# Optimization experiments

Hardware: AMD Instinct MI355X
Metric: run time of the kernel (lower is better)

Reference implementation:

```python
import jax, jax.numpy as jnp
import numpy as np

H, BS, NB, R, K = 2048, 128, 44, 64, 8   # hidden, block_size, num_blocks, basis_rank, top_k
B, S = 4, 2048
I = NB * BS                               # intermediate size = 5632


def setup_inputs() -> dict:
    key = jax.random.key(0)
    ks = jax.random.split(key, 10)
    N = B * S
    return {
        "hidden_states": jax.random.normal(ks[0], (B, S, H), jnp.float32),
        "active_idx": jax.random.randint(ks[1], (N, K), 0, NB, jnp.int32),
        "active_score": jax.random.uniform(ks[2], (N, K), dtype=jnp.float32),
        "gate_w": jax.random.normal(ks[3], (I, H), jnp.float32) * 0.02,
        "up_w": jax.random.normal(ks[4], (I, H), jnp.float32) * 0.02,
        "down_w": jax.random.normal(ks[5], (H, I), jnp.float32) * 0.02,
        "enc_w": jax.random.normal(ks[6], (R, H), jnp.float32) * 0.02,
        "enc_b": jnp.zeros((R,), jnp.float32),
        "decoder": jax.random.normal(ks[7], (NB, R, BS), jnp.float32) * 0.02,
        "basis_bias": jnp.zeros((NB, BS), jnp.float32),
        "comp_bias": jnp.zeros((H,), jnp.float32),
        "scale": jnp.array(1.0, jnp.float32),
    }


def reference(hidden_states, active_idx, active_score, gate_w, up_w, down_w,
              enc_w, enc_b, decoder, basis_bias, comp_bias, scale):
    Bb, Ss, Hh = hidden_states.shape
    N = Bb * Ss
    x = hidden_states.reshape(N, Hh)                          # [N, H]

    # routing weights: softmax over selected block scores (all idx valid here),
    # scattered into a dense per-token per-block weight map (duplicates accumulate)
    w = jax.nn.softmax(active_score, axis=-1)                 # [N, K]
    block_w = jnp.zeros((N, NB), x.dtype).at[
        jnp.arange(N)[:, None], active_idx].add(w)            # [N, NB]

    # gated SiLU MLP intermediate over all blocks (dense equivalent of the
    # per-token block gather-compute)
    act = jax.nn.silu(x @ gate_w.T) * (x @ up_w.T)            # [N, I]

    # low-rank basis compensation: latent -> per-block block_size channels
    latent = jax.nn.silu(x @ enc_w.T + enc_b)                 # [N, R]
    comp = jnp.einsum('nr,brc->nbc', latent, decoder) + basis_bias  # [N, NB, BS]

    act_b = act.reshape(N, NB, BS) + scale * comp             # [N, NB, BS]
    weighted = (act_b * block_w[:, :, None]).reshape(N, I)    # mask+weight inactive blocks to 0

    out = weighted @ down_w.T + comp_bias                     # scatter back via down proj
    return out.reshape(Bb, Ss, Hh)
```

## Files before the change

kernel.cpp:

```cpp
#include <hip/hip_runtime.h>

#define H_  2048
#define BS_ 128
#define NB_ 44
#define R_  64
#define K_  8
#define N_  8192
#define I_  5632
#define MT  64
#define TILES 32
#define GRID_AB (8 * 6 * TILES)

typedef __bf16 bf16x8 __attribute__((ext_vector_type(8)));
typedef float  f32x4  __attribute__((ext_vector_type(4)));

__device__ __forceinline__ unsigned short f2bf(float f) {
  unsigned int u = __float_as_uint(f);
  u = (u + 0x7FFFu + ((u >> 16) & 1u)) >> 16;
  return (unsigned short)u;
}
__device__ __forceinline__ float bf2f(unsigned short s) {
  return __uint_as_float(((unsigned int)s) << 16);
}
__device__ __forceinline__ bf16x8 ld8(const unsigned short* p) {
  uint4 v = *reinterpret_cast<const uint4*>(p);
  return __builtin_bit_cast(bf16x8, v);
}
__device__ __forceinline__ bf16x8 lds8(const char* p) {
  uint4 v = *reinterpret_cast<const uint4*>(p);
  return __builtin_bit_cast(bf16x8, v);
}
__device__ __forceinline__ void gl16(const void* g, void* l) {
  __builtin_amdgcn_global_load_lds(
      (const __attribute__((address_space(1))) char*)g,
      (__attribute__((address_space(3))) char*)l, 16, 0, 0);
}
#define WAIT_VM(n) do { asm volatile("s_waitcnt vmcnt(" #n ")" ::: "memory"); \
                        __builtin_amdgcn_sched_barrier(0); } while (0)
#define WAIT_LGKM0 do { asm volatile("s_waitcnt lgkmcnt(0)" ::: "memory"); \
                        __builtin_amdgcn_sched_barrier(0); } while (0)
#define SBAR __builtin_amdgcn_s_barrier()

__global__ void cvt_xgu(const float* __restrict__ x, const float* __restrict__ gw,
                        const float* __restrict__ uw, const float* __restrict__ ew,
                        const float* __restrict__ dw,
                        unsigned short* __restrict__ xb,
                        unsigned short* __restrict__ gwb,
                        unsigned short* __restrict__ uwb,
                        unsigned short* __restrict__ ewb,
                        unsigned short* __restrict__ dwb,
                        int do_down) {
  const int NX4 = N_ * H_ / 4;
  const int NG4 = I_ * H_ / 4;
  const int NE4 = R_ * H_ / 4;
  const int ND4 = H_ * I_ / 4;
  int total = NX4 + 2 * NG4 + NE4 + (do_down ? ND4 : 0);
  int stride = gridDim.x * blockDim.x;
  for (int i = blockIdx.x * blockDim.x + threadIdx.x; i < total; i += stride) {
    if (i < NX4 + 2 * NG4 + NE4) {
      const float4* s; ushort4* d; int j;
      if (i < NX4)                  { s = (const float4*)x;  d = (ushort4*)xb;  j = i; }
      else if (i < NX4 + NG4)       { s = (const float4*)gw; d = (ushort4*)gwb; j = i - NX4; }
      else if (i < NX4 + 2 * NG4)   { s = (const float4*)uw; d = (ushort4*)uwb; j = i - NX4 - NG4; }
      else                          { s = (const float4*)ew; d = (ushort4*)ewb; j = i - NX4 - 2 * NG4; }
      float4 v = s[j];
      ushort4 o; o.x = f2bf(v.x); o.y = f2bf(v.y); o.z = f2bf(v.z); o.w = f2bf(v.w);
      d[j] = o;
    } else {
      int j = i - (NX4 + 2 * NG4 + NE4);
      float4 v = ((const float4*)dw)[j];
      int flat = j * 4;
      int h = flat / I_;
      int rem = flat - h * I_;
      int b = rem >> 7, k = rem & 127;
      ushort4 o; o.x = f2bf(v.x); o.y = f2bf(v.y); o.z = f2bf(v.z); o.w = f2bf(v.w);
      *(ushort4*)(dwb + ((size_t)b * H_ + h) * BS_ + k) = o;
    }
  }
}

__global__ void cvt_down(const float* __restrict__ dw, unsigned short* __restrict__ dwb) {
  int total = H_ * I_ / 4;
  int stride = gridDim.x * blockDim.x;
  for (int i = blockIdx.x * blockDim.x + threadIdx.x; i < total; i += stride) {
    float4 v = ((const float4*)dw)[i];
    int flat = i * 4;
    int h = flat / I_;
    int rem = flat - h * I_;
    int b = rem >> 7, k = rem & 127;
    ushort4 o; o.x = f2bf(v.x); o.y = f2bf(v.y); o.z = f2bf(v.z); o.w = f2bf(v.w);
    *(ushort4*)(dwb + ((size_t)b * H_ + h) * BS_ + k) = o;
  }
}

__global__ void cvt_dec(const float* __restrict__ dec, unsigned short* __restrict__ decb) {
  int i = blockIdx.x * 256 + threadIdx.x;
  if (i >= NB_ * BS_ * R_) return;
  int b = i >> 13;
  int rem = i & 8191;
  int c = rem >> 6, r = rem & 63;
  decb[i] = f2bf(dec[(b << 13) + r * BS_ + c]);
}

__global__ void zero_counts(int* __restrict__ counts) {
  if (threadIdx.x < NB_) counts[threadIdx.x] = 0;
}

__global__ void prep_kernel(const float* __restrict__ score,
                            const int* __restrict__ aidx,
                            float* __restrict__ w_buf,
                            int* __restrict__ counts) {
  __shared__ int hist[NB_];
  int tid = threadIdx.x;
  if (tid < NB_) hist[tid] = 0;
  __syncthreads();
  int n = blockIdx.x * 256 + tid;
  float s[K_];
  float m = -1e30f;
#pragma unroll
  for (int k = 0; k < K_; k++) { s[k] = score[n * K_ + k]; m = fmaxf(m, s[k]); }
  float sum = 0.f;
#pragma unroll
  for (int k = 0; k < K_; k++) { s[k] = __expf(s[k] - m); sum += s[k]; }
  float inv = 1.f / sum;
#pragma unroll
  for (int k = 0; k < K_; k++) {
    w_buf[n * K_ + k] = s[k] * inv;
    atomicAdd(&hist[aidx[n * K_ + k]], 1);
  }
  __syncthreads();
  if (tid < NB_) atomicAdd(&counts[tid], hist[tid]);
}

__global__ void scan_kernel(const int* __restrict__ counts,
                            int* __restrict__ offsets,
                            int* __restrict__ cursors) {
  if (threadIdx.x == 0) {
    int acc = 0;
    for (int b = 0; b < NB_; b++) { offsets[b] = acc; cursors[b] = acc; acc += counts[b]; }
    offsets[NB_] = acc;
  }
}

__global__ void fill_kernel(const int* __restrict__ aidx,
                            const float* __restrict__ w_buf,
                            int* __restrict__ cursors,
                            int* __restrict__ tok_list,
                            float* __restrict__ wt_list,
                            int* __restrict__ inv) {
  int n = blockIdx.x * 256 + threadIdx.x;
#pragma unroll
  for (int k = 0; k < K_; k++) {
    int b = aidx[n * K_ + k];
    int pos = atomicAdd(&cursors[b], 1);
    tok_list[pos] = n;
    wt_list[pos] = w_buf[n * K_ + k];
    inv[n * K_ + k] = pos;
  }
}

__global__ __launch_bounds__(256) void latent_mfma(
    const unsigned short* __restrict__ xb,
    const unsigned short* __restrict__ ewb,
    const float* __restrict__ enc_b,
    unsigned short* __restrict__ lat) {
  __shared__ __align__(16) char smem[16384];
  int tid = threadIdx.x;
  int wv = tid >> 6, lane = tid & 63;
  int lo = lane & 15, hi = lane >> 4;
  int n0 = blockIdx.x * 64;

  int rowA = tid >> 2;
  int jA = (tid & 3) ^ ((rowA >> 1) & 3);
  const unsigned short* srcA = xb + (size_t)(n0 + rowA) * H_ + jA * 8;
  const unsigned short* srcB = ewb + (size_t)rowA * H_ + jA * 8;

  gl16(srcA, smem + wv * 1024);
  gl16(srcB, smem + 8192 + wv * 1024);

  f32x4 acc[4] = {};
  int cur = 0;
  for (int ks = 0; ks < H_; ks += 32) {
    if (ks + 32 < H_) {
      gl16(srcA + ks + 32, smem + (cur ^ 1) * 4096 + wv * 1024);
      gl16(srcB + ks + 32, smem + 8192 + (cur ^ 1) * 4096 + wv * 1024);
      WAIT_VM(2);
    } else {
      WAIT_VM(0);
    }
    SBAR;
    int rB = wv * 16 + lo;
    bf16x8 Bf = lds8(smem + 8192 + cur * 4096 + (rB * 4 + (hi ^ ((rB >> 1) & 3))) * 16);
#pragma unroll
    for (int m = 0; m < 4; m++) {
      int row = m * 16 + lo;
      bf16x8 Af = lds8(smem + cur * 4096 + (row * 4 + (hi ^ ((row >> 1) & 3))) * 16);
      acc[m] = __builtin_amdgcn_mfma_f32_16x16x32_bf16(Af, Bf, acc[m], 0, 0, 0);
    }
    WAIT_LGKM0;
    SBAR;
    cur ^= 1;
  }

  int r = wv * 16 + lo;
  float eb = enc_b[r];
#pragma unroll
  for (int m = 0; m < 4; m++) {
#pragma unroll
    for (int rg = 0; rg < 4; rg++) {
      int tok = n0 + m * 16 + hi * 4 + rg;
      float v = acc[m][rg] + eb;
      lat[(size_t)tok * R_ + r] = f2bf(v / (1.f + __expf(-v)));
    }
  }
}

__device__ __forceinline__ bool decode_bt(int p, int& b, int& tile) {
  b = (p & 7) + 8 * ((p >> 3) / TILES);
  tile = (p >> 3) % TILES;
  return b < NB_;
}

__global__ __launch_bounds__(256, 4) void gateup_kernel(
    const unsigned short* __restrict__ xb,
    const unsigned short* __restrict__ gwb,
    const unsigned short* __restrict__ uwb,
    const unsigned short* __restrict__ latb,
    const unsigned short* __restrict__ decb_all,
    const float* __restrict__ bbias,
    const float* __restrict__ scale_p,
    const int* __restrict__ counts,
    const int* __restrict__ offsets,
    const int* __restrict__ tok_list,
    const float* __restrict__ wt_list,
    unsigned short* __restrict__ actw) {
  int b, tile;
  if (!decode_bt(blockIdx.x, b, tile)) return;
  int cnt = counts[b];
  int base = tile * MT;
  if (base >= cnt) return;
  int off = offsets[b];

  __shared__ __align__(16) char smem[40960];

  int tid = threadIdx.x;
  int wv = tid >> 6, lane = tid & 63;
  int lo = lane & 15, hi = lane >> 4;

  int rowA = tid >> 2;
  int jA = (tid & 3) ^ ((rowA >> 1) & 3);
  int tokA = tok_list[off + min(base + rowA, cnt - 1)];
  const unsigned short* srcA = xb + (size_t)tokA * H_ + jA * 8;

  const unsigned short* gb = gwb + (size_t)b * BS_ * H_;
  const unsigned short* ub = uwb + (size_t)b * BS_ * H_;
  const unsigned short* srcG[2];
  const unsigned short* srcU[2];
#pragma unroll
  for (int s = 0; s < 2; s++) {
    int o = s * 256 + tid;
    int c = o >> 2;
    int j = (o & 3) ^ ((c >> 1) & 3);
    size_t e = (size_t)c * H_ + j * 8;
    srcG[s] = gb + e;
    srcU[s] = ub + e;
  }

  f32x4 accG[4][2] = {};
  f32x4 accU[4][2] = {};

  gl16(srcA, smem + wv * 1024);
#pragma unroll
  for (int s = 0; s < 2; s++) {
    gl16(srcG[s], smem + 8192 + s * 4096 + wv * 1024);
    gl16(srcU[s], smem + 24576 + s * 4096 + wv * 1024);
  }

  int cur = 0;
  for (int ks = 0; ks < H_; ks += 32) {
    if (ks + 32 < H_) {
      int nb_ = cur ^ 1;
      gl16(srcA + ks + 32, smem + nb_ * 4096 + wv * 1024);
#pragma unroll
      for (int s = 0; s < 2; s++) {
        gl16(srcG[s] + ks + 32, smem + 8192 + nb_ * 8192 + s * 4096 + wv * 1024);
        gl16(srcU[s] + ks + 32, smem + 24576 + nb_ * 8192 + s * 4096 + wv * 1024);
      }
      WAIT_VM(5);
    } else {
      WAIT_VM(0);
    }
    SBAR;
    bf16x8 Af[4];
#pragma unroll
    for (int m = 0; m < 4; m++) {
      int row = m * 16 + lo;
      int off16 = row * 4 + (hi ^ ((row >> 1) & 3));
      Af[m] = lds8(smem + cur * 4096 + off16 * 16);
    }
    bf16x8 Gf[2], Uf[2];
#pragma unroll
    for (int cf = 0; cf < 2; cf++) {
      int c = wv * 32 + cf * 16 + lo;
      int off16 = c * 4 + (hi ^ ((c >> 1) & 3));
      Gf[cf] = lds8(smem + 8192 + cur * 8192 + off16 * 16);
      Uf[cf] = lds8(smem + 24576 + cur * 8192 + off16 * 16);
    }
#pragma unroll
    for (int m = 0; m < 4; m++) {
#pragma unroll
      for (int cf = 0; cf < 2; cf++) {
        accG[m][cf] = __builtin_amdgcn_mfma_f32_16x16x32_bf16(Af[m], Gf[cf], accG[m][cf], 0, 0, 0);
        accU[m][cf] = __builtin_amdgcn_mfma_f32_16x16x32_bf16(Af[m], Uf[cf], accU[m][cf], 0, 0, 0);
      }
    }
    WAIT_LGKM0;
    SBAR;
    cur ^= 1;
  }

#pragma unroll
  for (int s = 0; s < 2; s++) {
    int o = s * 256 + tid;
    int r_ = o >> 3;
    int j = (o & 7) ^ (r_ & 7);
    int tokL = tok_list[off + min(base + r_, cnt - 1)];
    gl16(latb + (size_t)tokL * R_ + j * 8, smem + 24576 + s * 4096 + wv * 1024);
  }
  const unsigned short* decb = decb_all + (size_t)b * BS_ * R_;
#pragma unroll
  for (int s = 0; s < 4; s++) {
    int o = s * 256 + tid;
    int c = o >> 3;
    int j = (o & 7) ^ (c & 7);
    gl16(decb + (size_t)c * R_ + j * 8, smem + 8192 + s * 4096 + wv * 1024);
  }
  __syncthreads();

  f32x4 accC[4][2] = {};
#pragma unroll
  for (int kk = 0; kk < 2; kk++) {
    bf16x8 L[4];
#pragma unroll
    for (int m = 0; m < 4; m++) {
      int row = m * 16 + lo;
      int off16 = row * 8 + ((kk * 4 + hi) ^ (lo & 7));
      L[m] = lds8(smem + 24576 + off16 * 16);
    }
#pragma unroll
    for (int cf = 0; cf < 2; cf++) {
      int c = wv * 32 + cf * 16 + lo;
      int off16 = c * 8 + ((kk * 4 + hi) ^ (lo & 7));
      bf16x8 D = lds8(smem + 8192 + off16 * 16);
#pragma unroll
      for (int m = 0; m < 4; m++)
        accC[m][cf] = __builtin_amdgcn_mfma_f32_16x16x32_bf16(L[m], D, accC[m][cf], 0, 0, 0);
    }
  }

  float scal = scale_p[0];
  int cc[2] = { wv * 32 + lo, wv * 32 + 16 + lo };
  float bbv[2] = { bbias[b * BS_ + cc[0]], bbias[b * BS_ + cc[1]] };
#pragma unroll
  for (int m = 0; m < 4; m++) {
#pragma unroll
    for (int r = 0; r < 4; r++) {
      int t = m * 16 + hi * 4 + r;
      int g = base + t;
      if (g < cnt) {
        float wt = wt_list[off + g];
        unsigned short* dst = actw + (size_t)(off + g) * BS_;
#pragma unroll
        for (int cf = 0; cf < 2; cf++) {
          float gg = accG[m][cf][r];
          float uu = accU[m][cf][r];
          float act = (gg / (1.f + __expf(-gg))) * uu;
          dst[cc[cf]] = f2bf((act + scal * (accC[m][cf][r] + bbv[cf])) * wt);
        }
      }
    }
  }
}

__global__ __launch_bounds__(256) void down_kernel(
    const unsigned short* __restrict__ actw,
    const unsigned short* __restrict__ dwb,
    const int* __restrict__ counts,
    const int* __restrict__ offsets,
    unsigned short* __restrict__ partial,
    int hc0, int Hc) {
  int b, tile;
  if (!decode_bt(blockIdx.x, b, tile)) return;
  int cnt = counts[b];
  int base = tile * MT;
  if (base >= cnt) return;
  int off = offsets[b];

  __shared__ __align__(16) unsigned short a_lds[MT * BS_];
  __shared__ __align__(16) char b_lds[2][16384];
  int tid = threadIdx.x;
  int wv = tid >> 6, lane = tid & 63;
  int lo = lane & 15, hi = lane >> 4;

  for (int i = tid; i < MT * BS_ / 8; i += 256) {
    int t = i >> 4, cb = i & 15;
    int g = base + t;
    uint4 v = make_uint4(0, 0, 0, 0);
    if (g < cnt) v = *(const uint4*)(actw + (size_t)(off + g) * BS_ + cb * 8);
    *(uint4*)(&a_lds[t * BS_ + ((cb ^ (t & 7)) << 3)]) = v;
  }
  __syncthreads();

  bf16x8 Bf[4][4];
#pragma unroll
  for (int kst = 0; kst < 4; kst++)
#pragma unroll
    for (int sf = 0; sf < 4; sf++) {
      int t = sf * 16 + lo, cb = kst * 4 + hi;
      Bf[kst][sf] = ld8(&a_lds[t * BS_ + ((cb ^ (t & 7)) << 3)]);
    }

  const unsigned short* db = dwb + (size_t)b * H_ * BS_;
  int rs = tid >> 4;
  int jc = tid & 15;
  {
    const unsigned short* d0 = db + (size_t)hc0 * BS_;
#pragma unroll
    for (int s = 0; s < 4; s++) {
      int r = s * 16 + rs;
      int j = jc ^ (r & 15);
      gl16(d0 + (size_t)r * BS_ + j * 8, b_lds[0] + s * 4096 + wv * 1024);
    }
  }
  __syncthreads();

  int nit = Hc >> 6;
  int cur = 0;
  for (int it = 0; it < nit; it++) {
    if (it + 1 < nit) {
      const unsigned short* dn = db + (size_t)(hc0 + (it + 1) * 64) * BS_;
#pragma unroll
      for (int s = 0; s < 4; s++) {
        int r = s * 16 + rs;
        int j = jc ^ (r & 15);
        gl16(dn + (size_t)r * BS_ + j * 8, b_lds[cur ^ 1] + s * 4096 + wv * 1024);
      }
    }
    f32x4 acc[4] = {};
    int rl = wv * 16 + lo;
#pragma unroll
    for (int kst = 0; kst < 4; kst++) {
      int cb = kst * 4 + hi;
      bf16x8 Aw = lds8(b_lds[cur] + (rl * 16 + (cb ^ lo)) * 16);
#pragma unroll
      for (int sf = 0; sf < 4; sf++)
        acc[sf] = __builtin_amdgcn_mfma_f32_16x16x32_bf16(Aw, Bf[kst][sf], acc[sf], 0, 0, 0);
    }
    int hrel = it * 64 + wv * 16 + hi * 4;
#pragma unroll
    for (int sf = 0; sf < 4; sf++) {
      int g = base + sf * 16 + lo;
      if (g < cnt) {
        uint2 pk;
        pk.x = (unsigned int)f2bf(acc[sf][0]) | ((unsigned int)f2bf(acc[sf][1]) << 16);
        pk.y = (unsigned int)f2bf(acc[sf][2]) | ((unsigned int)f2bf(acc[sf][3]) << 16);
        *(uint2*)(partial + (size_t)(off + g) * Hc + hrel) = pk;
      }
    }
    __syncthreads();
    cur ^= 1;
  }
}

__global__ __launch_bounds__(256) void reduce_kernel(
    const unsigned short* __restrict__ partial,
    const int* __restrict__ inv,
    const float* __restrict__ cbias,
    float* __restrict__ out, int hc0, int Hc) {
  int wv = threadIdx.x >> 6, l = threadIdx.x & 63;
  int n = blockIdx.x * 4 + wv;
  int rows[K_];
#pragma unroll
  for (int k = 0; k < K_; k++) rows[k] = inv[n * K_ + k];
  for (int c0w = 0; c0w < Hc; c0w += 512) {
    int cw = c0w + l * 8;
    if (cw >= Hc) continue;
    float a[8] = {0.f, 0.f, 0.f, 0.f, 0.f, 0.f, 0.f, 0.f};
#pragma unroll
    for (int k = 0; k < K_; k++) {
      uint4 v = *(const uint4*)(partial + (size_t)rows[k] * Hc + cw);
      unsigned int w0 = v.x, w1 = v.y, w2 = v.z, w3 = v.w;
      a[0] += __uint_as_float(w0 << 16); a[1] += __uint_as_float(w0 & 0xFFFF0000u);
      a[2] += __uint_as_float(w1 << 16); a[3] += __uint_as_float(w1 & 0xFFFF0000u);
      a[4] += __uint_as_float(w2 << 16); a[5] += __uint_as_float(w2 & 0xFFFF0000u);
      a[6] += __uint_as_float(w3 << 16); a[7] += __uint_as_float(w3 & 0xFFFF0000u);
    }
    int h = hc0 + cw;
    float4 c0 = *(const float4*)(cbias + h);
    float4 c1 = *(const float4*)(cbias + h + 4);
    float4 o0 = make_float4(a[0] + c0.x, a[1] + c0.y, a[2] + c0.z, a[3] + c0.w);
    float4 o1 = make_float4(a[4] + c1.x, a[5] + c1.y, a[6] + c1.z, a[7] + c1.w);
    *(float4*)(out + (size_t)n * H_ + h) = o0;
    *(float4*)(out + (size_t)n * H_ + h + 4) = o1;
  }
}

extern "C" void kernel_launch(void* const* d_in, const int* in_sizes, int n_in,
                              void* d_out, int out_size, void* d_ws, size_t ws_size,
                              hipStream_t stream) {
  const float* x       = (const float*)d_in[0];
  const int*   aidx    = (const int*)d_in[1];
  const float* score   = (const float*)d_in[2];
  const float* gate_w  = (const float*)d_in[3];
  const float* up_w    = (const float*)d_in[4];
  const float* down_w  = (const float*)d_in[5];
  const float* enc_w   = (const float*)d_in[6];
  const float* enc_b   = (const float*)d_in[7];
  const float* decoder = (const float*)d_in[8];
  const float* bbias   = (const float*)d_in[9];
  const float* cbias   = (const float*)d_in[10];
  const float* scale   = (const float*)d_in[11];
  float* out = (float*)d_out;

  char* ws = (char*)d_ws;
  const size_t OFF_GWB  = 33554432ull;
  const size_t OFF_UWB  = 56623104ull;
  const size_t OFF_DEC  = 79691776ull;
  const size_t OFF_LATB = 80412672ull;
  const size_t OFF_ENCB = 81461248ull;
  const size_t OFF_WBUF = 81723392ull;
  const size_t OFF_TOK  = 81985536ull;
  const size_t OFF_WT   = 82247680ull;
  const size_t OFF_INV  = 82509824ull;
  const size_t OFF_CNT  = 82771968ull;
  const size_t OFF_ACTW = 82772992ull;
  const size_t BASE_END = 99550208ull;
  const size_t DWB_SZ   = 23068672ull;

  unsigned short* xb   = (unsigned short*)(ws);
  unsigned short* gwb  = (unsigned short*)(ws + OFF_GWB);
  unsigned short* uwb  = (unsigned short*)(ws + OFF_UWB);
  unsigned short* decb = (unsigned short*)(ws + OFF_DEC);
  unsigned short* latb = (unsigned short*)(ws + OFF_LATB);
  unsigned short* ewb  = (unsigned short*)(ws + OFF_ENCB);
  float* w_buf         = (float*)(ws + OFF_WBUF);
  int*   tok_list      = (int*)(ws + OFF_TOK);
  float* wt_list       = (float*)(ws + OFF_WT);
  int*   inv           = (int*)(ws + OFF_INV);
  int*   counts        = (int*)(ws + OFF_CNT);
  int*   offsets       = counts + 64;
  int*   cursors       = counts + 128;
  unsigned short* actw = (unsigned short*)(ws + OFF_ACTW);

  int Hc; unsigned short* dwb; unsigned short* partial; bool early_down;
  if      (ws_size >= BASE_END + DWB_SZ + 131072ull * 512) Hc = 512;
  else if (ws_size >= BASE_END + DWB_SZ + 131072ull * 256) Hc = 256;
  else Hc = 0;
  if (Hc) {
    early_down = true;
    dwb = (unsigned short*)(ws + BASE_END);
    partial = (unsigned short*)(ws + BASE_END + DWB_SZ);
  } else {
    early_down = false;
    Hc = 256;
    dwb = gwb;
    partial = (unsigned short*)ws;
  }
  int nch = H_ / Hc;

  cvt_xgu<<<2048, 256, 0, stream>>>(x, gate_w, up_w, enc_w, down_w,
                                    xb, gwb, uwb, ewb, dwb, early_down ? 1 : 0);
  cvt_dec<<<(NB_ * BS_ * R_ + 255) / 256, 256, 0, stream>>>(decoder, decb);
  zero_counts<<<1, 64, 0, stream>>>(counts);
  prep_kernel<<<N_ / 256, 256, 0, stream>>>(score, aidx, w_buf, counts);
  scan_kernel<<<1, 64, 0, stream>>>(counts, offsets, cursors);
  fill_kernel<<<N_ / 256, 256, 0, stream>>>(aidx, w_buf, cursors, tok_list, wt_list, inv);
  latent_mfma<<<N_ / 64, 256, 0, stream>>>(xb, ewb, enc_b, latb);
  gateup_kernel<<<GRID_AB, 256, 0, stream>>>(xb, gwb, uwb, latb, decb, bbias, scale,
                                             counts, offsets, tok_list, wt_list, actw);
  if (!early_down) cvt_down<<<2048, 256, 0, stream>>>(down_w, dwb);
  for (int c = 0; c < nch; c++) {
    down_kernel<<<GRID_AB, 256, 0, stream>>>(actw, dwb, counts, offsets, partial, c * Hc, Hc);
    reduce_kernel<<<N_ / 4, 256, 0, stream>>>(partial, inv, cbias, out, c * Hc, Hc);
  }
}
```

Before: 575.1 us.

## Triple-buffer activation tile in gate/up loop and allow larger down-proj chunk

The gate/up GEMM loop now keeps three LDS buffers for the gathered activation rows and prefetches them two K-steps ahead, while the weight tiles stay double-buffered. The aim is to hide the latency of the scattered token-row loads behind more MFMA work. This grows LDS per block and lowers the launch-bounds occupancy hint from 4 to 3 blocks. Separately, the host now picks a 1024-wide down-projection chunk when the workspace is large enough, which may change the partial-buffer layout and how much work each pass covers.

```diff
diff --git a/kernel.cpp b/kernel.cpp
--- a/kernel.cpp
+++ b/kernel.cpp
@@ -221,7 +221,7 @@
   return b < NB_;
 }
 
-__global__ __launch_bounds__(256, 4) void gateup_kernel(
+__global__ __launch_bounds__(256, 3) void gateup_kernel(
     const unsigned short* __restrict__ xb,
     const unsigned short* __restrict__ gwb,
     const unsigned short* __restrict__ uwb,
@@ -241,7 +241,7 @@
   if (base >= cnt) return;
   int off = offsets[b];
 
-  __shared__ __align__(16) char smem[40960];
+  __shared__ __align__(16) char smem[45056];
 
   int tid = threadIdx.x;
   int wv = tid >> 6, lane = tid & 63;
@@ -269,22 +269,31 @@
   f32x4 accG[4][2] = {};
   f32x4 accU[4][2] = {};
 
+#pragma unroll
+  for (int s = 0; s < 2; s++) {
+    gl16(srcG[s], smem + 12288 + s * 4096 + wv * 1024);
+    gl16(srcU[s], smem + 28672 + s * 4096 + wv * 1024);
+  }
   gl16(srcA, smem + wv * 1024);
-#pragma unroll
-  for (int s = 0; s < 2; s++) {
-    gl16(srcG[s], smem + 8192 + s * 4096 + wv * 1024);
-    gl16(srcU[s], smem + 24576 + s * 4096 + wv * 1024);
-  }
-
-  int cur = 0;
-  for (int ks = 0; ks < H_; ks += 32) {
-    if (ks + 32 < H_) {
-      int nb_ = cur ^ 1;
-      gl16(srcA + ks + 32, smem + nb_ * 4096 + wv * 1024);
+  gl16(srcA + 32, smem + 4096 + wv * 1024);
+
+  int acur = 0, awr = 2;
+  for (int it = 0; it < 64; ++it) {
+    int ks = it * 32;
+    if (it < 62) {
+      int gu = (it + 1) & 1;
 #pragma unroll
       for (int s = 0; s < 2; s++) {
-        gl16(srcG[s] + ks + 32, smem + 8192 + nb_ * 8192 + s * 4096 + wv * 1024);
-        gl16(srcU[s] + ks + 32, smem + 24576 + nb_ * 8192 + s * 4096 + wv * 1024);
+        gl16(srcG[s] + ks + 32, smem + 12288 + gu * 8192 + s * 4096 + wv * 1024);
+        gl16(srcU[s] + ks + 32, smem + 28672 + gu * 8192 + s * 4096 + wv * 1024);
+      }
+      gl16(srcA + ks + 64, smem + awr * 4096 + wv * 1024);
+      WAIT_VM(6);
+    } else if (it == 62) {
+#pragma unroll
+      for (int s = 0; s < 2; s++) {
+        gl16(srcG[s] + ks + 32, smem + 12288 + 8192 + s * 4096 + wv * 1024);
+        gl16(srcU[s] + ks + 32, smem + 28672 + 8192 + s * 4096 + wv * 1024);
       }
       WAIT_VM(5);
     } else {
@@ -296,15 +305,16 @@
     for (int m = 0; m < 4; m++) {
       int row = m * 16 + lo;
       int off16 = row * 4 + (hi ^ ((row >> 1) & 3));
-      Af[m] = lds8(smem + cur * 4096 + off16 * 16);
+      Af[m] = lds8(smem + acur * 4096 + off16 * 16);
     }
     bf16x8 Gf[2], Uf[2];
+    int gub = it & 1;
 #pragma unroll
     for (int cf = 0; cf < 2; cf++) {
       int c = wv * 32 + cf * 16 + lo;
       int off16 = c * 4 + (hi ^ ((c >> 1) & 3));
-      Gf[cf] = lds8(smem + 8192 + cur * 8192 + off16 * 16);
-      Uf[cf] = lds8(smem + 24576 + cur * 8192 + off16 * 16);
+      Gf[cf] = lds8(smem + 12288 + gub * 8192 + off16 * 16);
+      Uf[cf] = lds8(smem + 28672 + gub * 8192 + off16 * 16);
     }
 #pragma unroll
     for (int m = 0; m < 4; m++) {
@@ -316,7 +326,8 @@
     }
     WAIT_LGKM0;
     SBAR;
-    cur ^= 1;
+    acur = (acur == 2) ? 0 : acur + 1;
+    awr  = (awr  == 2) ? 0 : awr  + 1;
   }
 
 #pragma unroll
@@ -325,7 +336,7 @@
     int r_ = o >> 3;
     int j = (o & 7) ^ (r_ & 7);
     int tokL = tok_list[off + min(base + r_, cnt - 1)];
-    gl16(latb + (size_t)tokL * R_ + j * 8, smem + 24576 + s * 4096 + wv * 1024);
+    gl16(latb + (size_t)tokL * R_ + j * 8, smem + 28672 + s * 4096 + wv * 1024);
   }
   const unsigned short* decb = decb_all + (size_t)b * BS_ * R_;
 #pragma unroll
@@ -333,7 +344,7 @@
     int o = s * 256 + tid;
     int c = o >> 3;
     int j = (o & 7) ^ (c & 7);
-    gl16(decb + (size_t)c * R_ + j * 8, smem + 8192 + s * 4096 + wv * 1024);
+    gl16(decb + (size_t)c * R_ + j * 8, smem + 12288 + s * 4096 + wv * 1024);
   }
   __syncthreads();
 
@@ -345,13 +356,13 @@
     for (int m = 0; m < 4; m++) {
       int row = m * 16 + lo;
       int off16 = row * 8 + ((kk * 4 + hi) ^ (lo & 7));
-      L[m] = lds8(smem + 24576 + off16 * 16);
+      L[m] = lds8(smem + 28672 + off16 * 16);
     }
 #pragma unroll
     for (int cf = 0; cf < 2; cf++) {
       int c = wv * 32 + cf * 16 + lo;
       int off16 = c * 8 + ((kk * 4 + hi) ^ (lo & 7));
-      bf16x8 D = lds8(smem + 8192 + off16 * 16);
+      bf16x8 D = lds8(smem + 12288 + off16 * 16);
 #pragma unroll
       for (int m = 0; m < 4; m++)
         accC[m][cf] = __builtin_amdgcn_mfma_f32_16x16x32_bf16(L[m], D, accC[m][cf], 0, 0, 0);
@@ -553,8 +564,9 @@
   unsigned short* actw = (unsigned short*)(ws + OFF_ACTW);
 
   int Hc; unsigned short* dwb; unsigned short* partial; bool early_down;
-  if      (ws_size >= BASE_END + DWB_SZ + 131072ull * 512) Hc = 512;
-  else if (ws_size >= BASE_END + DWB_SZ + 131072ull * 256) Hc = 256;
+  if      (ws_size >= BASE_END + DWB_SZ + 131072ull * 1024) Hc = 1024;
+  else if (ws_size >= BASE_END + DWB_SZ + 131072ull * 512)  Hc = 512;
+  else if (ws_size >= BASE_END + DWB_SZ + 131072ull * 256)  Hc = 256;
   else Hc = 0;
   if (Hc) {
     early_down = true;
```

Measured after the change: 557.7 us. -3.0%, faster.

## Enlarge gate/up tile to 128 tokens with 512-thread blocks in a 2x4 wave grid

Applied to the files above, without the earlier changes.

The gate/up kernel now processes 128 tokens per block with 8 waves arranged as 2 row groups by 4 column groups, so each loaded gate/up weight tile is reused across twice as many tokens. The grid shrinks to half as many tiles per block and shared memory grows to 48KB. This cuts redundant weight loads from global memory, at the cost of fewer blocks (less parallelism when per-block token counts are uneven) and higher LDS use per block, which may lower occupancy.

```diff
diff --git a/kernel.cpp b/kernel.cpp
--- a/kernel.cpp
+++ b/kernel.cpp
@@ -10,6 +10,9 @@
 #define MT  64
 #define TILES 32
 #define GRID_AB (8 * 6 * TILES)
+#define MT2 128
+#define TILES_GU 16
+#define GRID_GU (8 * 6 * TILES_GU)
 
 typedef __bf16 bf16x8 __attribute__((ext_vector_type(8)));
 typedef float  f32x4  __attribute__((ext_vector_type(4)));
@@ -220,8 +223,13 @@
   tile = (p >> 3) % TILES;
   return b < NB_;
 }
-
-__global__ __launch_bounds__(256, 4) void gateup_kernel(
+__device__ __forceinline__ bool decode_bt_gu(int p, int& b, int& tile) {
+  b = (p & 7) + 8 * ((p >> 3) / TILES_GU);
+  tile = (p >> 3) % TILES_GU;
+  return b < NB_;
+}
+
+__global__ __launch_bounds__(512, 4) void gateup_kernel(
     const unsigned short* __restrict__ xb,
     const unsigned short* __restrict__ gwb,
     const unsigned short* __restrict__ uwb,
@@ -235,17 +243,18 @@
     const float* __restrict__ wt_list,
     unsigned short* __restrict__ actw) {
   int b, tile;
-  if (!decode_bt(blockIdx.x, b, tile)) return;
+  if (!decode_bt_gu(blockIdx.x, b, tile)) return;
   int cnt = counts[b];
-  int base = tile * MT;
+  int base = tile * MT2;
   if (base >= cnt) return;
   int off = offsets[b];
 
-  __shared__ __align__(16) char smem[40960];
+  __shared__ __align__(16) char smem[49152];
 
   int tid = threadIdx.x;
   int wv = tid >> 6, lane = tid & 63;
   int lo = lane & 15, hi = lane >> 4;
+  int wr = wv >> 2, wc = wv & 3;
 
   int rowA = tid >> 2;
   int jA = (tid & 3) ^ ((rowA >> 1) & 3);
@@ -254,57 +263,45 @@
 
   const unsigned short* gb = gwb + (size_t)b * BS_ * H_;
   const unsigned short* ub = uwb + (size_t)b * BS_ * H_;
-  const unsigned short* srcG[2];
-  const unsigned short* srcU[2];
-#pragma unroll
-  for (int s = 0; s < 2; s++) {
-    int o = s * 256 + tid;
-    int c = o >> 2;
-    int j = (o & 3) ^ ((c >> 1) & 3);
-    size_t e = (size_t)c * H_ + j * 8;
-    srcG[s] = gb + e;
-    srcU[s] = ub + e;
-  }
+  int cS = tid >> 2;
+  int jS = (tid & 3) ^ ((cS >> 1) & 3);
+  const unsigned short* srcG = gb + (size_t)cS * H_ + jS * 8;
+  const unsigned short* srcU = ub + (size_t)cS * H_ + jS * 8;
 
   f32x4 accG[4][2] = {};
   f32x4 accU[4][2] = {};
 
   gl16(srcA, smem + wv * 1024);
-#pragma unroll
-  for (int s = 0; s < 2; s++) {
-    gl16(srcG[s], smem + 8192 + s * 4096 + wv * 1024);
-    gl16(srcU[s], smem + 24576 + s * 4096 + wv * 1024);
-  }
-
-  int cur = 0;
-  for (int ks = 0; ks < H_; ks += 32) {
-    if (ks + 32 < H_) {
-      int nb_ = cur ^ 1;
-      gl16(srcA + ks + 32, smem + nb_ * 4096 + wv * 1024);
-#pragma unroll
-      for (int s = 0; s < 2; s++) {
-        gl16(srcG[s] + ks + 32, smem + 8192 + nb_ * 8192 + s * 4096 + wv * 1024);
-        gl16(srcU[s] + ks + 32, smem + 24576 + nb_ * 8192 + s * 4096 + wv * 1024);
-      }
-      WAIT_VM(5);
+  gl16(srcG, smem + 16384 + wv * 1024);
+  gl16(srcU, smem + 32768 + wv * 1024);
+
+  for (int it = 0; it < 64; ++it) {
+    int ks = it * 32;
+    if (it < 63) {
+      int nb_ = (it + 1) & 1;
+      gl16(srcA + ks + 32, smem + nb_ * 8192 + wv * 1024);
+      gl16(srcG + ks + 32, smem + 16384 + nb_ * 8192 + wv * 1024);
+      gl16(srcU + ks + 32, smem + 32768 + nb_ * 8192 + wv * 1024);
+      WAIT_VM(3);
     } else {
       WAIT_VM(0);
     }
     SBAR;
+    int cur = it & 1;
     bf16x8 Af[4];
 #pragma unroll
     for (int m = 0; m < 4; m++) {
-      int row = m * 16 + lo;
+      int row = wr * 64 + m * 16 + lo;
       int off16 = row * 4 + (hi ^ ((row >> 1) & 3));
-      Af[m] = lds8(smem + cur * 4096 + off16 * 16);
+      Af[m] = lds8(smem + cur * 8192 + off16 * 16);
     }
     bf16x8 Gf[2], Uf[2];
 #pragma unroll
     for (int cf = 0; cf < 2; cf++) {
-      int c = wv * 32 + cf * 16 + lo;
+      int c = wc * 32 + cf * 16 + lo;
       int off16 = c * 4 + (hi ^ ((c >> 1) & 3));
-      Gf[cf] = lds8(smem + 8192 + cur * 8192 + off16 * 16);
-      Uf[cf] = lds8(smem + 24576 + cur * 8192 + off16 * 16);
+      Gf[cf] = lds8(smem + 16384 + cur * 8192 + off16 * 16);
+      Uf[cf] = lds8(smem + 32768 + cur * 8192 + off16 * 16);
     }
 #pragma unroll
     for (int m = 0; m < 4; m++) {
@@ -316,24 +313,23 @@
     }
     WAIT_LGKM0;
     SBAR;
-    cur ^= 1;
   }
 
 #pragma unroll
   for (int s = 0; s < 2; s++) {
-    int o = s * 256 + tid;
+    int o = s * 512 + tid;
     int r_ = o >> 3;
     int j = (o & 7) ^ (r_ & 7);
     int tokL = tok_list[off + min(base + r_, cnt - 1)];
-    gl16(latb + (size_t)tokL * R_ + j * 8, smem + 24576 + s * 4096 + wv * 1024);
+    gl16(latb + (size_t)tokL * R_ + j * 8, smem + 32768 + s * 8192 + wv * 1024);
   }
   const unsigned short* decb = decb_all + (size_t)b * BS_ * R_;
 #pragma unroll
-  for (int s = 0; s < 4; s++) {
-    int o = s * 256 + tid;
+  for (int s = 0; s < 2; s++) {
+    int o = s * 512 + tid;
     int c = o >> 3;
     int j = (o & 7) ^ (c & 7);
-    gl16(decb + (size_t)c * R_ + j * 8, smem + 8192 + s * 4096 + wv * 1024);
+    gl16(decb + (size_t)c * R_ + j * 8, smem + 16384 + s * 8192 + wv * 1024);
   }
   __syncthreads();
 
@@ -343,15 +339,15 @@
     bf16x8 L[4];
 #pragma unroll
     for (int m = 0; m < 4; m++) {
-      int row = m * 16 + lo;
-      int off16 = row * 8 + ((kk * 4 + hi) ^ (lo & 7));
-      L[m] = lds8(smem + 24576 + off16 * 16);
+      int row = wr * 64 + m * 16 + lo;
+      int off16 = row * 8 + ((kk * 4 + hi) ^ (row & 7));
+      L[m] = lds8(smem + 32768 + off16 * 16);
     }
 #pragma unroll
     for (int cf = 0; cf < 2; cf++) {
-      int c = wv * 32 + cf * 16 + lo;
-      int off16 = c * 8 + ((kk * 4 + hi) ^ (lo & 7));
-      bf16x8 D = lds8(smem + 8192 + off16 * 16);
+      int c = wc * 32 + cf * 16 + lo;
+      int off16 = c * 8 + ((kk * 4 + hi) ^ (c & 7));
+      bf16x8 D = lds8(smem + 16384 + off16 * 16);
 #pragma unroll
       for (int m = 0; m < 4; m++)
         accC[m][cf] = __builtin_amdgcn_mfma_f32_16x16x32_bf16(L[m], D, accC[m][cf], 0, 0, 0);
@@ -359,13 +355,13 @@
   }
 
   float scal = scale_p[0];
-  int cc[2] = { wv * 32 + lo, wv * 32 + 16 + lo };
+  int cc[2] = { wc * 32 + lo, wc * 32 + 16 + lo };
   float bbv[2] = { bbias[b * BS_ + cc[0]], bbias[b * BS_ + cc[1]] };
 #pragma unroll
   for (int m = 0; m < 4; m++) {
 #pragma unroll
     for (int r = 0; r < 4; r++) {
-      int t = m * 16 + hi * 4 + r;
+      int t = wr * 64 + m * 16 + hi * 4 + r;
       int g = base + t;
       if (g < cnt) {
         float wt = wt_list[off + g];
@@ -576,7 +572,7 @@
   scan_kernel<<<1, 64, 0, stream>>>(counts, offsets, cursors);
   fill_kernel<<<N_ / 256, 256, 0, stream>>>(aidx, w_buf, cursors, tok_list, wt_list, inv);
   latent_mfma<<<N_ / 64, 256, 0, stream>>>(xb, ewb, enc_b, latb);
-  gateup_kernel<<<GRID_AB, 256, 0, stream>>>(xb, gwb, uwb, latb, decb, bbias, scale,
+  gateup_kernel<<<GRID_GU, 512, 0, stream>>>(xb, gwb, uwb, latb, decb, bbias, scale,
                                              counts, offsets, tok_list, wt_list, actw);
   if (!early_down) cvt_down<<<2048, 256, 0, stream>>>(down_w, dwb);
   for (int c = 0; c < nch; c++) {
```

Result: faster. 548.5 us (-4.6%).
